# Optimization experiments

Hardware: AMD Instinct MI355X
Metric: run time of the kernel (lower is better)

## Reference

```python
import jax, jax.numpy as jnp
import numpy as np

# dims
B, LP, CIN, AUX = 8, 1024, 64, 32
COUT, OUT_LEN = 64, 512
DM, DI, NS, PH, NH = 1024, 2048, 16, 64, 32  # d_model, d_inner, d_state, headdim, n_heads
NL, PATCH, KPRE, KCONV = 4, 8, 5, 4
GG, KH, CHUNK = 8, 2048, 64  # kan grid, kan hidden, chunk_size
DIN = 2 * DI + 2 * NS + NH   # in_proj output: z, xBC, dt
CONV_DIM = DI + 2 * NS


def _conv1d(x, w, b, stride, pad_l, pad_r, groups=1):
    # x: [B, C, L], w: [O, I/groups, K]
    y = jax.lax.conv_general_dilated(x, w, (stride,), [(pad_l, pad_r)],
                                     dimension_numbers=("NCH", "OIH", "NCH"),
                                     feature_group_count=groups)
    return y + b[None, :, None]


def _rmsnorm(x, w):
    return x * jax.lax.rsqrt(jnp.mean(x * x, axis=-1, keepdims=True) + 1e-5) * w


def _mamba(u, in_w, conv_w, conv_b, A_log, Dh, dt_bias, out_w):
    # Mamba2-style selective SSM block (bias-free projections, causal depthwise conv).
    Bs, L, _ = u.shape
    zxbcdt = jnp.einsum("bld,ed->ble", u, in_w)  # [B,L,DIN]
    z = zxbcdt[..., :DI]
    xBC = zxbcdt[..., DI:DI + CONV_DIM]
    dt = jax.nn.softplus(zxbcdt[..., DI + CONV_DIM:] + dt_bias)  # [B,L,NH]
    xBC = jax.nn.silu(_conv1d(xBC.transpose(0, 2, 1), conv_w, conv_b, 1, KCONV - 1, 0,
                              groups=CONV_DIM)).transpose(0, 2, 1)
    xh = xBC[..., :DI].reshape(Bs, L, NH, PH)
    Bm = xBC[..., DI:DI + NS]   # [B,L,NS]
    Cm = xBC[..., DI + NS:]     # [B,L,NS]
    dA = jnp.exp(-jnp.exp(A_log) * dt)  # [B,L,NH]

    def step(s, t):
        x_t, B_t, C_t, dA_t, dt_t = t
        s = s * dA_t[:, :, None, None] + jnp.einsum("bhp,bn,bh->bhpn", x_t, B_t, dt_t)
        return s, jnp.einsum("bhpn,bn->bhp", s, C_t)

    s0 = jnp.zeros((Bs, NH, PH, NS), u.dtype)
    xs = (xh.transpose(1, 0, 2, 3), Bm.transpose(1, 0, 2), Cm.transpose(1, 0, 2),
          dA.transpose(1, 0, 2), dt.transpose(1, 0, 2))
    _, ys = jax.lax.scan(step, s0, xs)  # ys: [L,B,NH,PH]
    y = ys.transpose(1, 0, 2, 3) + xh * Dh[None, None, :, None]
    y = y.reshape(Bs, L, DI) * jax.nn.silu(z)
    return jnp.einsum("ble,de->bld", y, out_w)


def _kan(x, log_bw, base_w, base_b, spline_w):
    # Gaussian-basis KAN layer: base Linear + spline Linear over RBF expansion.
    grid = jnp.linspace(-2.0, 2.0, GG)
    bw = jnp.exp(log_bw)[None] + 1e-6                 # [1,in,1]
    basis = jnp.exp(-((x[..., None] - grid[None, None, :]) ** 2) / (2.0 * bw * bw))
    return x @ base_w.T + base_b + basis.reshape(x.shape[0], -1) @ spline_w.T


def setup_inputs() -> dict:
    ks = iter(jax.random.split(jax.random.key(0), 64))
    nrm = lambda shape, s=0.02: jax.random.normal(next(ks), shape, jnp.float32) * s
    inp = {"x_prefix": jax.random.normal(next(ks), (B, LP, CIN), jnp.float32),
           "y_aux": jax.random.normal(next(ks), (B, AUX), jnp.float32),
           "pre_conv_w": nrm((DM, CIN, KPRE), 0.1), "pre_conv_b": jnp.zeros((DM,)),
           "patch_w": nrm((DM, DM, PATCH), 0.05), "patch_b": jnp.zeros((DM,))}
    for pre in ("fwd", "bwd"):
        inp[pre + "_norm_w"] = jnp.ones((NL, DM))
        inp[pre + "_in_w"] = nrm((NL, DIN, DM))
        inp[pre + "_conv_w"] = nrm((NL, CONV_DIM, 1, KCONV), 0.1)
        inp[pre + "_conv_b"] = jnp.zeros((NL, CONV_DIM))
        inp[pre + "_A_log"] = jnp.zeros((NL, NH))
        inp[pre + "_D"] = jnp.ones((NL, NH))
        inp[pre + "_dt_bias"] = nrm((NL, NH), 0.5)
        inp[pre + "_out_w"] = nrm((NL, DM, DI))
    inp.update(aux_w=nrm((DM, AUX)), aux_b=jnp.zeros((DM,)),
               kan1_log_bw=jnp.zeros((3 * DM, 1)), kan1_base_w=nrm((KH, 3 * DM)),
               kan1_base_b=jnp.zeros((KH,)), kan1_spline_w=nrm((KH, 3 * DM * GG), 0.005),
               kan2_log_bw=jnp.zeros((KH, 1)), kan2_base_w=nrm((DM, KH)),
               kan2_base_b=jnp.zeros((DM,)), kan2_spline_w=nrm((DM, KH * GG), 0.005),
               shared_w=nrm((DM, DM)), shared_b=jnp.zeros((DM,)),
               heads_w=nrm((COUT, OUT_LEN, DM)), heads_b=jnp.zeros((COUT, OUT_LEN)))
    return inp


def reference(x_prefix, y_aux, pre_conv_w, pre_conv_b, patch_w, patch_b,
              fwd_norm_w, fwd_in_w, fwd_conv_w, fwd_conv_b, fwd_A_log, fwd_D, fwd_dt_bias, fwd_out_w,
              bwd_norm_w, bwd_in_w, bwd_conv_w, bwd_conv_b, bwd_A_log, bwd_D, bwd_dt_bias, bwd_out_w,
              aux_w, aux_b, kan1_log_bw, kan1_base_w, kan1_base_b, kan1_spline_w,
              kan2_log_bw, kan2_base_w, kan2_base_b, kan2_spline_w,
              shared_w, shared_b, heads_w, heads_b):
    # encode_prefix
    x = jax.nn.silu(_conv1d(x_prefix.transpose(0, 2, 1), pre_conv_w, pre_conv_b, 1, KPRE // 2, KPRE // 2))
    x = _conv1d(x, patch_w, patch_b, PATCH, 0, 0).transpose(0, 2, 1)  # [B, 128, DM]
    rem = x.shape[1] % CHUNK
    if rem:
        x = jnp.pad(x, ((0, 0), (0, CHUNK - rem), (0, 0)))
    h_f, h_b = x, x[:, ::-1]
    for i in range(NL):
        h_f = h_f + _mamba(_rmsnorm(h_f, fwd_norm_w[i]), fwd_in_w[i], fwd_conv_w[i], fwd_conv_b[i],
                           fwd_A_log[i], fwd_D[i], fwd_dt_bias[i], fwd_out_w[i])
        h_b = h_b + _mamba(_rmsnorm(h_b, bwd_norm_w[i]), bwd_in_w[i], bwd_conv_w[i], bwd_conv_b[i],
                           bwd_A_log[i], bwd_D[i], bwd_dt_bias[i], bwd_out_w[i])
    ctx = jnp.concatenate([h_f.mean(1), h_b[:, ::-1].mean(1)], axis=-1)  # [B, 2*DM]
    # fusion + heads
    aux = jax.nn.silu(y_aux @ aux_w.T + aux_b)
    fused = jnp.concatenate([ctx, aux], axis=-1)  # [B, 3*DM]
    fused = jax.nn.silu(_kan(fused, kan1_log_bw, kan1_base_w, kan1_base_b, kan1_spline_w))
    fused = jax.nn.silu(_kan(fused, kan2_log_bw, kan2_base_w, kan2_base_b, kan2_spline_w))
    fused = jax.nn.silu(fused @ shared_w.T + shared_b)
    # all channel heads fused into one batched GEMM: [B, OUT_LEN, COUT]
    return jnp.einsum("bd,cld->blc", fused, heads_w) + heads_b.T[None]
```

## Files before the change

### kernel.cpp

```cpp
#include <hip/hip_runtime.h>
#include <hip/hip_bf16.h>
#include <math.h>

#define B_    8
#define LP_   1024
#define CIN_  64
#define DM_   1024
#define DI_   2048
#define NS_   16
#define PH_   64
#define NH_   32
#define NL_   4
#define GG_   8
#define KH_   2048
#define DIN_  4160
#define NPAD_ 4224
#define CONVD_ 2080
#define L_    128
#define R_    1024
#define OUTL_ 512
#define COUT_ 64

typedef __bf16 bf16x8 __attribute__((ext_vector_type(8)));
typedef float f32x4 __attribute__((ext_vector_type(4)));
typedef unsigned short ushort;

__device__ __forceinline__ float silu_f(float x) { return x / (1.0f + expf(-x)); }

__device__ __forceinline__ ushort f2bu(float x) {
    union { __hip_bfloat16 h; ushort u; } c; c.h = __float2bfloat16(x); return c.u;
}
__device__ __forceinline__ float bu2f(ushort u) {
    union { ushort u; __hip_bfloat16 h; } c; c.u = u; return __bfloat162float(c.h);
}

__device__ __forceinline__ void gload_lds16(const void* g, void* l) {
    __builtin_amdgcn_global_load_lds((const __attribute__((address_space(1))) unsigned int*)g,
                                     (__attribute__((address_space(3))) unsigned int*)l, 16, 0, 0);
}

__device__ __forceinline__ float merge2(float a, float b, int mask, int lane) {
    float x = (lane & mask) ? b : a;
    float y = (lane & mask) ? a : b;
    return x + __shfl_xor(y, mask);
}
__device__ __forceinline__ float reduce8(float* a, int lane) {
    float c0 = merge2(a[0], a[1], 1, lane);
    float c1 = merge2(a[2], a[3], 1, lane);
    float c2 = merge2(a[4], a[5], 1, lane);
    float c3 = merge2(a[6], a[7], 1, lane);
    float d0 = merge2(c0, c1, 2, lane);
    float d1 = merge2(c2, c3, 2, lane);
    float e  = merge2(d0, d1, 4, lane);
    e += __shfl_xor(e, 8);
    e += __shfl_xor(e, 16);
    e += __shfl_xor(e, 32);
    return e;
}

#define PREP_W1 327680
#define PREP_W2 8388608
#define PREP_W3 2621440
__global__ __launch_bounds__(256) void k_prep(const float* __restrict__ pre_w, const float* __restrict__ patch_w,
                                              const float* __restrict__ xp,
                                              __hip_bfloat16* __restrict__ wpreT, __hip_bfloat16* __restrict__ wpatchT,
                                              __hip_bfloat16* __restrict__ Apre) {
    int idx = blockIdx.x * 256 + threadIdx.x;
    if (idx < PREP_W1) {
        int d = idx / 320, kk = idx % 320;
        int kp = kk >> 6, c = kk & 63;
        wpreT[idx] = __float2bfloat16(pre_w[(d * CIN_ + c) * 5 + kp]);
    } else if (idx < PREP_W1 + PREP_W2) {
        int i = idx - PREP_W1;
        int d = i >> 13, kk = i & 8191;
        int kp = kk >> 10, din = kk & 1023;
        wpatchT[i] = __float2bfloat16(patch_w[((size_t)d << 13) + din * 8 + kp]);
    } else if (idx < PREP_W1 + PREP_W2 + PREP_W3) {
        int i = idx - PREP_W1 - PREP_W2;
        int kk = i % 320; int r = i / 320;
        int l = r & 1023, b = r >> 10;
        int kp = kk >> 6, c = kk & 63;
        int lp = l + kp - 2;
        float v = 0.f;
        if (lp >= 0 && lp < LP_) v = xp[((size_t)b * LP_ + lp) * CIN_ + c];
        Apre[i] = __float2bfloat16(v);
    }
}

#define CVT_IN_T4  1081344
#define CVT_OUT_T4 524288
#define CVT_PER    1605632
__global__ __launch_bounds__(256) void k_cvt_all(const float* __restrict__ in0, const float* __restrict__ in1,
                                                 const float* __restrict__ o0, const float* __restrict__ o1,
                                                 __hip_bfloat16* __restrict__ wBBa, __hip_bfloat16* __restrict__ wOBa) {
    int i = blockIdx.x * 256 + threadIdx.x;
    if (i >= 8 * CVT_PER) return;
    int ld = i / CVT_PER;
    int r = i - ld * CVT_PER;
    int l = ld >> 1, d = ld & 1;
    const float* inw  = (d ? in1 : in0) + (size_t)l * DIN_ * DM_;
    const float* outw = (d ? o1 : o0) + (size_t)l * DM_ * DI_;
    if (r < CVT_IN_T4) {
        int idx = r * 4; int row = idx >> 10;
        __hip_bfloat16* dst = wBBa + (size_t)ld * NPAD_ * 1024 + idx;
        if (row < DIN_) {
            float4 v = *(const float4*)(inw + idx);
            dst[0] = __float2bfloat16(v.x); dst[1] = __float2bfloat16(v.y);
            dst[2] = __float2bfloat16(v.z); dst[3] = __float2bfloat16(v.w);
        } else {
            dst[0] = __float2bfloat16(0.f); dst[1] = __float2bfloat16(0.f);
            dst[2] = __float2bfloat16(0.f); dst[3] = __float2bfloat16(0.f);
        }
    } else {
        int idx = (r - CVT_IN_T4) * 4;
        __hip_bfloat16* dst = wOBa + (size_t)ld * 2048 * 1024 + idx;
        float4 v = *(const float4*)(outw + idx);
        dst[0] = __float2bfloat16(v.x); dst[1] = __float2bfloat16(v.y);
        dst[2] = __float2bfloat16(v.z); dst[3] = __float2bfloat16(v.w);
    }
}

template<int BM, int BN>
__global__ __launch_bounds__(256) void k_gemm_mfma(
    const ushort* __restrict__ A, const ushort* __restrict__ B,
    const float* __restrict__ bias,
    float* __restrict__ Cf, __hip_bfloat16* __restrict__ Cb,
    int Kc, int ldk, int ldc, int Nstore, int act, int nsplit,
    long sA, long sB, long sC)
{
    constexpr int BK = 32;
    constexpr int WM = BM / 2, WN = BN / 2;
    constexpr int MR = WM / 16, NR = WN / 16;
    constexpr int ACH = BM * 4, BCH = BN * 4;
    __shared__ ushort sAs[2][BM * BK];
    __shared__ ushort sBs[2][BN * BK];
    int tid = threadIdx.x;
    int lane = tid & 63, w = tid >> 6;
    int wr = w >> 1, wc = w & 1;
    int z = blockIdx.z;
    int dir = z / nsplit, ks = z - dir * nsplit;
    int kbase = ks * Kc;
    int m0 = blockIdx.y * BM, n0 = blockIdx.x * BN;
    const ushort* Az = A + (size_t)dir * sA + kbase;
    const ushort* Bz = B + (size_t)dir * sB + kbase;

    auto STAGE = [&](int buf, int k0) {
        #pragma unroll
        for (int c = tid; c < ACH; c += 256) {
            int row = c >> 2, col = (c & 3) * 8;
            gload_lds16(Az + (size_t)(m0 + row) * ldk + k0 + col, (char*)&sAs[buf][0] + c * 16);
        }
        #pragma unroll
        for (int c = tid; c < BCH; c += 256) {
            int row = c >> 2, col = (c & 3) * 8;
            gload_lds16(Bz + (size_t)(n0 + row) * ldk + k0 + col, (char*)&sBs[buf][0] + c * 16);
        }
    };

    f32x4 acc[MR][NR] = {};
    const int NT = Kc / BK;
    STAGE(0, 0);
    __syncthreads();
    int cur = 0;
    for (int t = 0; t < NT; ++t) {
        if (t + 1 < NT) STAGE(cur ^ 1, (t + 1) * BK);
        bf16x8 af[MR], bfr[NR];
        #pragma unroll
        for (int m = 0; m < MR; ++m)
            af[m] = *(const bf16x8*)&sAs[cur][(wr * WM + m * 16 + (lane & 15)) * BK + (lane >> 4) * 8];
        #pragma unroll
        for (int n = 0; n < NR; ++n)
            bfr[n] = *(const bf16x8*)&sBs[cur][(wc * WN + n * 16 + (lane & 15)) * BK + (lane >> 4) * 8];
        #pragma unroll
        for (int m = 0; m < MR; ++m)
            #pragma unroll
            for (int n = 0; n < NR; ++n)
                acc[m][n] = __builtin_amdgcn_mfma_f32_16x16x32_bf16(af[m], bfr[n], acc[m][n], 0, 0, 0);
        __syncthreads();
        cur ^= 1;
    }
    #pragma unroll
    for (int m = 0; m < MR; ++m) {
        int row = m0 + wr * WM + m * 16 + (lane >> 4) * 4;
        #pragma unroll
        for (int n = 0; n < NR; ++n) {
            int col = n0 + wc * WN + n * 16 + (lane & 15);
            if (col < Nstore) {
                if (act == 2) {
                    float* Cfz = Cf + (size_t)z * sC;
                    #pragma unroll
                    for (int j = 0; j < 4; ++j)
                        Cfz[(size_t)(row + j) * ldc + col] = acc[m][n][j];
                } else {
                    __hip_bfloat16* Cbz = Cb + (size_t)dir * sC;
                    float bv = bias ? bias[col] : 0.f;
                    #pragma unroll
                    for (int j = 0; j < 4; ++j) {
                        float v = acc[m][n][j] + bv;
                        if (act == 1) v = silu_f(v);
                        Cbz[(size_t)(row + j) * ldc + col] = __float2bfloat16(v);
                    }
                }
            }
        }
    }
}

__global__ __launch_bounds__(256) void k_patch_fin_rms(const float* __restrict__ part, const float* __restrict__ bias,
                                                       const float* __restrict__ w0, const float* __restrict__ w1,
                                                       float* __restrict__ hf, float* __restrict__ hb,
                                                       __hip_bfloat16* __restrict__ uB) {
    int r = blockIdx.x;
    int t = threadIdx.x;
    int c = t * 4;
    float4 o = *(const float4*)(bias + c);
    #pragma unroll
    for (int s = 0; s < 8; ++s) {
        float4 v = *(const float4*)(part + (size_t)s * 1048576 + ((size_t)r << 10) + c);
        o.x += v.x; o.y += v.y; o.z += v.z; o.w += v.w;
    }
    *(float4*)(hf + ((size_t)r << 10) + c) = o;
    int rb = r ^ 127;
    *(float4*)(hb + ((size_t)rb << 10) + c) = o;
    float ss = o.x * o.x + o.y * o.y + o.z * o.z + o.w * o.w;
    #pragma unroll
    for (int of = 32; of; of >>= 1) ss += __shfl_xor(ss, of);
    __shared__ float sred[4];
    if ((t & 63) == 0) sred[t >> 6] = ss;
    __syncthreads();
    float tot = sred[0] + sred[1] + sred[2] + sred[3];
    float scale = rsqrtf(tot * (1.0f / DM_) + 1e-5f);
    float4 wf = *(const float4*)(w0 + c);
    float4 wb = *(const float4*)(w1 + c);
    __hip_bfloat16* uf = uB + ((size_t)r << 10) + c;
    __hip_bfloat16* ub = uB + ((size_t)(1024 + rb) << 10) + c;
    uf[0] = __float2bfloat16(o.x * scale * wf.x); uf[1] = __float2bfloat16(o.y * scale * wf.y);
    uf[2] = __float2bfloat16(o.z * scale * wf.z); uf[3] = __float2bfloat16(o.w * scale * wf.w);
    ub[0] = __float2bfloat16(o.x * scale * wb.x); ub[1] = __float2bfloat16(o.y * scale * wb.y);
    ub[2] = __float2bfloat16(o.z * scale * wb.z); ub[3] = __float2bfloat16(o.w * scale * wb.w);
}

template<bool DO_RMS>
__global__ __launch_bounds__(256) void k_oproj_fin_rms(const float* __restrict__ part,
                                                       const float* __restrict__ w0, const float* __restrict__ w1,
                                                       float* __restrict__ h, __hip_bfloat16* __restrict__ uB) {
    int row = blockIdx.x;
    int t = threadIdx.x;
    int c = t * 4;
    const float* p = part + (size_t)(row >> 10) * 4194304 + (size_t)(row & 1023) * 1024 + c;
    float4 o = *(const float4*)(h + ((size_t)row << 10) + c);
    #pragma unroll
    for (int s = 0; s < 4; ++s) {
        float4 v = *(const float4*)(p + (size_t)s * 1048576);
        o.x += v.x; o.y += v.y; o.z += v.z; o.w += v.w;
    }
    *(float4*)(h + ((size_t)row << 10) + c) = o;
    if (DO_RMS) {
        float ss = o.x * o.x + o.y * o.y + o.z * o.z + o.w * o.w;
        #pragma unroll
        for (int of = 32; of; of >>= 1) ss += __shfl_xor(ss, of);
        __shared__ float sred[4];
        if ((t & 63) == 0) sred[t >> 6] = ss;
        __syncthreads();
        float tot = sred[0] + sred[1] + sred[2] + sred[3];
        float scale = rsqrtf(tot * (1.0f / DM_) + 1e-5f);
        const float* w = (row >> 10) ? w1 : w0;
        float4 wv = *(const float4*)(w + c);
        __hip_bfloat16* u = uB + ((size_t)row << 10) + c;
        u[0] = __float2bfloat16(o.x * scale * wv.x); u[1] = __float2bfloat16(o.y * scale * wv.y);
        u[2] = __float2bfloat16(o.z * scale * wv.z); u[3] = __float2bfloat16(o.w * scale * wv.w);
    }
}

__global__ __launch_bounds__(256) void k_scan(const __hip_bfloat16* __restrict__ zx,
                                              const float* __restrict__ cw0, const float* __restrict__ cw1,
                                              const float* __restrict__ cb0, const float* __restrict__ cb1,
                                              const float* __restrict__ dtb0, const float* __restrict__ dtb1,
                                              const float* __restrict__ al0, const float* __restrict__ al1,
                                              const float* __restrict__ D0, const float* __restrict__ D1,
                                              __hip_bfloat16* __restrict__ ys) {
    __shared__ float xs[L_ * PH_];
    __shared__ float Bsh[L_ * NS_];
    __shared__ float Csh[L_ * NS_];
    __shared__ float dts[L_];
    __shared__ float dAs[L_];
    int bx = blockIdx.x;
    int dir = bx >> 8, b = (bx >> 5) & 7, h = bx & 31;
    const __hip_bfloat16* zxd = zx + (size_t)dir * 1024 * DIN_;
    const float* cw = dir ? cw1 : cw0;
    const float* cb = dir ? cb1 : cb0;
    const float* dt_bias = dir ? dtb1 : dtb0;
    const float* A_log   = dir ? al1 : al0;
    const float* Dh      = dir ? D1 : D0;
    __hip_bfloat16* ysd  = ys + (size_t)dir * 1024 * DI_;
    int t = threadIdx.x;
    for (int i = t; i < 2048; i += 256) {
        int l = i >> 4, p4 = i & 15;
        int cc = h * PH_ + p4 * 4;
        float a0 = cb[cc + 0], a1 = cb[cc + 1], a2 = cb[cc + 2], a3 = cb[cc + 3];
        #pragma unroll
        for (int k = 0; k < 4; ++k) {
            int lp = l - 3 + k;
            if (lp >= 0) {
                ushort4 raw = *(const ushort4*)(zxd + (size_t)(b * L_ + lp) * DIN_ + DI_ + cc);
                a0 += bu2f(raw.x) * cw[(cc + 0) * 4 + k];
                a1 += bu2f(raw.y) * cw[(cc + 1) * 4 + k];
                a2 += bu2f(raw.z) * cw[(cc + 2) * 4 + k];
                a3 += bu2f(raw.w) * cw[(cc + 3) * 4 + k];
            }
        }
        float* xp = &xs[l * PH_ + p4 * 4];
        xp[0] = silu_f(a0); xp[1] = silu_f(a1); xp[2] = silu_f(a2); xp[3] = silu_f(a3);
    }
    for (int i = t; i < 1024; i += 256) {
        int l = i >> 3, q4 = i & 7;
        int cc = DI_ + q4 * 4;
        float a0 = cb[cc + 0], a1 = cb[cc + 1], a2 = cb[cc + 2], a3 = cb[cc + 3];
        #pragma unroll
        for (int k = 0; k < 4; ++k) {
            int lp = l - 3 + k;
            if (lp >= 0) {
                ushort4 raw = *(const ushort4*)(zxd + (size_t)(b * L_ + lp) * DIN_ + DI_ + cc);
                a0 += bu2f(raw.x) * cw[(cc + 0) * 4 + k];
                a1 += bu2f(raw.y) * cw[(cc + 1) * 4 + k];
                a2 += bu2f(raw.z) * cw[(cc + 2) * 4 + k];
                a3 += bu2f(raw.w) * cw[(cc + 3) * 4 + k];
            }
        }
        float r0 = silu_f(a0), r1 = silu_f(a1), r2 = silu_f(a2), r3 = silu_f(a3);
        if (q4 < 4) {
            float* bp = &Bsh[l * NS_ + q4 * 4];
            bp[0] = r0; bp[1] = r1; bp[2] = r2; bp[3] = r3;
        } else {
            float* cp = &Csh[l * NS_ + (q4 - 4) * 4];
            cp[0] = r0; cp[1] = r1; cp[2] = r2; cp[3] = r3;
        }
    }
    if (t < L_) {
        float v = bu2f(*(const ushort*)(zxd + (size_t)(b * L_ + t) * DIN_ + 4128 + h)) + dt_bias[h];
        float sp = v > 20.f ? v : log1pf(expf(v));
        dts[t] = sp;
        dAs[t] = expf(-expf(A_log[h]) * sp);
    }
    __syncthreads();
    int p = t >> 2, n0 = (t & 3) * 4;
    float Dv = Dh[h];
    float s0 = 0.f, s1 = 0.f, s2 = 0.f, s3 = 0.f;
    for (int l = 0; l < L_; ++l) {
        float x = xs[l * 64 + p];
        float dAv = dAs[l];
        float xdt = x * dts[l];
        s0 = s0 * dAv + xdt * Bsh[l * 16 + n0 + 0];
        s1 = s1 * dAv + xdt * Bsh[l * 16 + n0 + 1];
        s2 = s2 * dAv + xdt * Bsh[l * 16 + n0 + 2];
        s3 = s3 * dAv + xdt * Bsh[l * 16 + n0 + 3];
        float cp = s0 * Csh[l * 16 + n0 + 0] + s1 * Csh[l * 16 + n0 + 1]
                 + s2 * Csh[l * 16 + n0 + 2] + s3 * Csh[l * 16 + n0 + 3];
        cp += __shfl_xor(cp, 1);
        cp += __shfl_xor(cp, 2);
        if ((t & 3) == 0) xs[l * 64 + p] = cp + x * Dv;
    }
    __syncthreads();
    for (int i = t; i < L_ * PH_; i += 256) {
        int l = i >> 6, pp = i & 63;
        float z = bu2f(*(const ushort*)(zxd + (size_t)(b * L_ + l) * DIN_ + h * PH_ + pp));
        ysd[((size_t)(b * L_ + l)) * DI_ + h * PH_ + pp] = __float2bfloat16(xs[i] * silu_f(z));
    }
}

__global__ __launch_bounds__(256) void k_meanctx_aux(const float* __restrict__ hf, const float* __restrict__ hb,
                                                     const float* __restrict__ y_aux, const float* __restrict__ aux_w,
                                                     const float* __restrict__ aux_b, float* __restrict__ fused) {
    int bx = blockIdx.x;
    int t = threadIdx.x;
    if (bx < 64) {
        int b = bx >> 3, ch = bx & 7;
        int d4 = t & 31, lg = t >> 5;
        int d = ch * 128 + d4 * 4;
        float4 sf = {0,0,0,0}, sb = {0,0,0,0};
        for (int l = lg; l < L_; l += 8) {
            float4 a = *(const float4*)(hf + ((size_t)b * L_ + l) * DM_ + d);
            float4 c = *(const float4*)(hb + ((size_t)b * L_ + l) * DM_ + d);
            sf.x += a.x; sf.y += a.y; sf.z += a.z; sf.w += a.w;
            sb.x += c.x; sb.y += c.y; sb.z += c.z; sb.w += c.w;
        }
        __shared__ float rf[8][128], rb[8][128];
        *(float4*)&rf[lg][d4 * 4] = sf;
        *(float4*)&rb[lg][d4 * 4] = sb;
        __syncthreads();
        if (t < 128) {
            float s1 = 0.f, s2 = 0.f;
            #pragma unroll
            for (int g = 0; g < 8; ++g) { s1 += rf[g][t]; s2 += rb[g][t]; }
            fused[b * 3072 + ch * 128 + t] = s1 * (1.f / L_);
            fused[b * 3072 + DM_ + ch * 128 + t] = s2 * (1.f / L_);
        }
    } else {
        int j = (bx - 64) * 256 + t;
        if (j >= DM_) return;
        for (int b = 0; b < B_; ++b) {
            float acc = aux_b[j];
            for (int a = 0; a < 32; ++a) acc += y_aux[b * 32 + a] * aux_w[j * 32 + a];
            fused[b * 3072 + 2 * DM_ + j] = silu_f(acc);
        }
    }
}

__global__ __launch_bounds__(256) void k_basis(const float* __restrict__ x, const float* __restrict__ log_bw,
                                               float* __restrict__ basis, int Din) {
    int idx = blockIdx.x * 256 + threadIdx.x;
    if (idx >= 8 * Din) return;
    int d = idx % Din;
    float xv = x[idx];
    float bw = expf(log_bw[d]) + 1e-6f;
    float inv = 1.0f / (2.0f * bw * bw);
    #pragma unroll
    for (int g = 0; g < GG_; ++g) {
        float gg = -2.0f + g * (4.0f / 7.0f);
        float df = xv - gg;
        basis[(size_t)idx * GG_ + g] = expf(-df * df * inv);
    }
}

template<int MODE>
__global__ __launch_bounds__(256) void k_dotk(const float* __restrict__ Wsp, const float* __restrict__ Xsp, int Ksp,
                                              const float* __restrict__ Wb, const float* __restrict__ Xb, int Kb,
                                              const float* __restrict__ bias, float* __restrict__ out,
                                              int nsp, int nch, int Dout) {
    __shared__ float sX[8][1024];
    int ch = blockIdx.y;
    bool sp = (ch < nsp);
    const float* W = sp ? Wsp : Wb;
    const float* X = sp ? Xsp : Xb;
    int K = sp ? Ksp : Kb;
    int k0 = (sp ? ch : ch - nsp) * 1024;
    int tid = threadIdx.x;
    for (int i = tid; i < 2048; i += 256) {
        int b = i >> 8, kk = (i & 255) * 4;
        *(float4*)&sX[b][kk] = *(const float4*)(X + (size_t)b * K + k0 + kk);
    }
    __syncthreads();
    int wv = tid >> 6, lane = tid & 63;
    int rowBase = blockIdx.x * 32 + wv * 8;
    for (int j = 0; j < 8; ++j) {
        int row = rowBase + j;
        const float* wr = W + (size_t)row * K + k0;
        float acc[8] = {};
        #pragma unroll
        for (int it = 0; it < 4; ++it) {
            int k = it * 256 + lane * 4;
            float4 wvv = *(const float4*)(wr + k);
            #pragma unroll
            for (int b = 0; b < 8; ++b) {
                float4 xv = *(const float4*)&sX[b][k];
                acc[b] += wvv.x * xv.x + wvv.y * xv.y + wvv.z * xv.z + wvv.w * xv.w;
            }
        }
        float e = reduce8(acc, lane);
        if (lane < 8) {
            if (MODE == 0) {
                out[((size_t)row * nch + ch) * 8 + lane] = e;
            } else if (MODE == 1) {
                out[(size_t)lane * Dout + row] = silu_f(e + bias[row]);
            } else {
                int c = row >> 9, l = row & 511;
                out[((size_t)lane * OUTL_ + l) * COUT_ + c] = e + bias[row];
            }
        }
    }
}

__global__ __launch_bounds__(256) void k_fin1_basis2(const float* __restrict__ partial, const float* __restrict__ bb,
                                                     const float* __restrict__ k2_lbw,
                                                     float* __restrict__ k1, float* __restrict__ bas2) {
    int row = blockIdx.x * 256 + threadIdx.x;
    if (row >= 2048) return;
    float bbv = bb[row];
    float lb = expf(k2_lbw[row]) + 1e-6f;
    float inv = 1.0f / (2.0f * lb * lb);
    #pragma unroll
    for (int b = 0; b < 8; ++b) {
        float s = bbv;
        #pragma unroll
        for (int c = 0; c < 27; ++c) s += partial[((size_t)row * 27 + c) * 8 + b];
        float v = silu_f(s);
        k1[(size_t)b * 2048 + row] = v;
        #pragma unroll
        for (int g = 0; g < GG_; ++g) {
            float gg = -2.0f + g * (4.0f / 7.0f);
            float df = v - gg;
            bas2[((size_t)b * 2048 + row) * GG_ + g] = expf(-df * df * inv);
        }
    }
}

template<int NCH>
__global__ __launch_bounds__(256) void k_dot_fin(const float* __restrict__ partial, const float* __restrict__ base_b,
                                                 float* __restrict__ out, int Dout) {
    int row = blockIdx.x * 256 + threadIdx.x;
    if (row >= Dout) return;
    float bb = base_b[row];
    #pragma unroll
    for (int b = 0; b < 8; ++b) {
        float s = bb;
        #pragma unroll
        for (int c = 0; c < NCH; ++c) s += partial[((size_t)row * NCH + c) * 8 + b];
        out[(size_t)b * Dout + row] = silu_f(s);
    }
}

extern "C" void kernel_launch(void* const* d_in, const int* in_sizes, int n_in,
                              void* d_out, int out_size, void* d_ws, size_t ws_size,
                              hipStream_t stream) {
    const float* x_prefix = (const float*)d_in[0];
    const float* y_aux    = (const float*)d_in[1];
    const float* pre_w    = (const float*)d_in[2];
    const float* pre_b    = (const float*)d_in[3];
    const float* patch_w  = (const float*)d_in[4];
    const float* patch_b  = (const float*)d_in[5];
    const float* norm_w[2] = {(const float*)d_in[6],  (const float*)d_in[14]};
    const float* in_w[2]   = {(const float*)d_in[7],  (const float*)d_in[15]};
    const float* conv_w[2] = {(const float*)d_in[8],  (const float*)d_in[16]};
    const float* conv_b[2] = {(const float*)d_in[9],  (const float*)d_in[17]};
    const float* A_log[2]  = {(const float*)d_in[10], (const float*)d_in[18]};
    const float* Dvec[2]   = {(const float*)d_in[11], (const float*)d_in[19]};
    const float* dt_b[2]   = {(const float*)d_in[12], (const float*)d_in[20]};
    const float* out_w[2]  = {(const float*)d_in[13], (const float*)d_in[21]};
    const float* aux_w = (const float*)d_in[22];
    const float* aux_b = (const float*)d_in[23];
    const float* k1_lbw = (const float*)d_in[24];
    const float* k1_bw  = (const float*)d_in[25];
    const float* k1_bb  = (const float*)d_in[26];
    const float* k1_sw  = (const float*)d_in[27];
    const float* k2_lbw = (const float*)d_in[28];
    const float* k2_bw  = (const float*)d_in[29];
    const float* k2_bb  = (const float*)d_in[30];
    const float* k2_sw  = (const float*)d_in[31];
    const float* sh_w = (const float*)d_in[32];
    const float* sh_b = (const float*)d_in[33];
    const float* hw   = (const float*)d_in[34];
    const float* hbias= (const float*)d_in[35];
    float* ws = (float*)d_ws;
    float* out = (float*)d_out;

    const size_t o_ApreB   = 0;
    const size_t o_wpreTB  = 1310720;
    const size_t o_x1B     = 1474560;
    const size_t o_wpatchTB= 5668864;
    const size_t o_uB   = 0;
    const size_t o_zxB  = 1048576;
    const size_t o_ysB  = 5308416;
    const size_t o_hf   = 9863168;
    const size_t o_hb   = 10911744;
    const size_t o_wBBa = 11960320;
    const size_t o_wOBa = 29261824;
    const size_t o_spart= 37650432;
    const size_t total_f = 46039040;
    const size_t o_f1   = 0;
    const size_t o_bas1 = 24576;
    const size_t o_k1   = 221184;
    const size_t o_bas2 = 237568;
    const size_t o_k2   = 368640;
    const size_t o_f4   = 376832;
    const size_t o_part = 385024;
    if (ws_size < total_f * sizeof(float)) return;

    __hip_bfloat16* ApreB   = (__hip_bfloat16*)(ws + o_ApreB);
    __hip_bfloat16* wpreTB  = (__hip_bfloat16*)(ws + o_wpreTB);
    __hip_bfloat16* x1B     = (__hip_bfloat16*)(ws + o_x1B);
    __hip_bfloat16* wpatchTB= (__hip_bfloat16*)(ws + o_wpatchTB);
    __hip_bfloat16* uB      = (__hip_bfloat16*)(ws + o_uB);
    __hip_bfloat16* zxB     = (__hip_bfloat16*)(ws + o_zxB);
    __hip_bfloat16* ysB     = (__hip_bfloat16*)(ws + o_ysB);
    __hip_bfloat16* wBBa    = (__hip_bfloat16*)(ws + o_wBBa);
    __hip_bfloat16* wOBa    = (__hip_bfloat16*)(ws + o_wOBa);
    float* hf = ws + o_hf;
    float* hb = ws + o_hb;

    k_cvt_all<<<50176, 256, 0, stream>>>(in_w[0], in_w[1], out_w[0], out_w[1], wBBa, wOBa);
    k_prep<<<44288, 256, 0, stream>>>(pre_w, patch_w, x_prefix, wpreTB, wpatchTB, ApreB);
    k_gemm_mfma<128,128><<<dim3(8, 64, 1), 256, 0, stream>>>(
        (const ushort*)ApreB, (const ushort*)wpreTB, pre_b, nullptr, x1B,
        320, 320, 1024, 1024, 1, 1, 0, 0, 0);
    k_gemm_mfma<128,128><<<dim3(8, 8, 8), 256, 0, stream>>>(
        (const ushort*)x1B, (const ushort*)wpatchTB, nullptr, ws + o_spart, nullptr,
        1024, 8192, 1024, 1024, 2, 8, 0, 0, (long)1024 * 1024);
    k_patch_fin_rms<<<1024, 256, 0, stream>>>(ws + o_spart, patch_b, norm_w[0], norm_w[1], hf, hb, uB);

    for (int i = 0; i < NL_; ++i) {
        k_gemm_mfma<128,128><<<dim3(33, 8, 2), 256, 0, stream>>>(
            (const ushort*)uB, (const ushort*)(wBBa + (size_t)i * 2 * NPAD_ * 1024), nullptr, nullptr, zxB,
            1024, 1024, DIN_, DIN_, 0, 1, (long)1024 * 1024, (long)NPAD_ * 1024, (long)1024 * DIN_);
        k_scan<<<512, 256, 0, stream>>>(zxB,
            conv_w[0] + (size_t)i * CONVD_ * 4, conv_w[1] + (size_t)i * CONVD_ * 4,
            conv_b[0] + (size_t)i * CONVD_, conv_b[1] + (size_t)i * CONVD_,
            dt_b[0] + i * NH_, dt_b[1] + i * NH_, A_log[0] + i * NH_, A_log[1] + i * NH_,
            Dvec[0] + i * NH_, Dvec[1] + i * NH_, ysB);
        k_gemm_mfma<128,128><<<dim3(8, 8, 8), 256, 0, stream>>>(
            (const ushort*)ysB, (const ushort*)(wOBa + (size_t)i * 2 * 2048 * 1024), nullptr, ws + o_spart, nullptr,
            512, 2048, 1024, 1024, 2, 4, (long)1024 * 2048, (long)2048 * 1024, (long)1024 * 1024);
        if (i + 1 < NL_) {
            k_oproj_fin_rms<true><<<2048, 256, 0, stream>>>(ws + o_spart,
                norm_w[0] + (size_t)(i + 1) * DM_, norm_w[1] + (size_t)(i + 1) * DM_, hf, uB);
        } else {
            k_oproj_fin_rms<false><<<2048, 256, 0, stream>>>(ws + o_spart, nullptr, nullptr, hf, nullptr);
        }
    }

    k_meanctx_aux<<<68, 256, 0, stream>>>(hf, hb, y_aux, aux_w, aux_b, ws + o_f1);
    k_basis<<<96, 256, 0, stream>>>(ws + o_f1, k1_lbw, ws + o_bas1, 3072);
    k_dotk<0><<<dim3(64, 27), 256, 0, stream>>>(k1_sw, ws + o_bas1, 24576, k1_bw, ws + o_f1, 3072,
                                                nullptr, ws + o_part, 24, 27, 2048);
    k_fin1_basis2<<<8, 256, 0, stream>>>(ws + o_part, k1_bb, k2_lbw, ws + o_k1, ws + o_bas2);
    k_dotk<0><<<dim3(32, 18), 256, 0, stream>>>(k2_sw, ws + o_bas2, 16384, k2_bw, ws + o_k1, 2048,
                                                nullptr, ws + o_part, 16, 18, 1024);
    k_dot_fin<18><<<4, 256, 0, stream>>>(ws + o_part, k2_bb, ws + o_k2, 1024);
    k_dotk<1><<<dim3(32, 1), 256, 0, stream>>>(nullptr, nullptr, 0, sh_w, ws + o_k2, 1024,
                                               sh_b, ws + o_f4, 0, 1, 1024);
    k_dotk<2><<<dim3(1024, 1), 256, 0, stream>>>(nullptr, nullptr, 0, hw, ws + o_f4, 1024,
                                                 hbias, out, 0, 1, 32768);
}
```

Baseline: 883.0 us.

## Use 8-wave GEMM blocks and merge weight-conversion and prep kernels

The MFMA GEMM now runs 512 threads per block, with eight waves in a 2x4 layout and 64x32 per-wave sub-tiles in place of four waves covering 64x64 each. This lowers accumulator registers per wave and adds waves per CU to hide latency, at the cost of more LDS-read traffic per block. The separate fp32-to-bf16 weight conversion and prep kernels are fused into one launch to save a kernel launch and its tail. The GEMM change touches every projection in the model.

```diff
diff --git a/kernel.cpp b/kernel.cpp
--- a/kernel.cpp
+++ b/kernel.cpp
@@ -58,14 +58,49 @@
     return e;
 }
 
+#define CVT_IN_T4  1081344
+#define CVT_OUT_T4 524288
+#define CVT_PER    1605632
+#define CVT_TOT    12845056
 #define PREP_W1 327680
 #define PREP_W2 8388608
 #define PREP_W3 2621440
-__global__ __launch_bounds__(256) void k_prep(const float* __restrict__ pre_w, const float* __restrict__ patch_w,
-                                              const float* __restrict__ xp,
-                                              __hip_bfloat16* __restrict__ wpreT, __hip_bfloat16* __restrict__ wpatchT,
-                                              __hip_bfloat16* __restrict__ Apre) {
-    int idx = blockIdx.x * 256 + threadIdx.x;
+#define PREP_TOT 11337728
+__global__ __launch_bounds__(256) void k_cvt_prep(
+    const float* __restrict__ in0, const float* __restrict__ in1,
+    const float* __restrict__ o0, const float* __restrict__ o1,
+    __hip_bfloat16* __restrict__ wBBa, __hip_bfloat16* __restrict__ wOBa,
+    const float* __restrict__ pre_w, const float* __restrict__ patch_w, const float* __restrict__ xp,
+    __hip_bfloat16* __restrict__ wpreT, __hip_bfloat16* __restrict__ wpatchT, __hip_bfloat16* __restrict__ Apre)
+{
+    int gi = blockIdx.x * 256 + threadIdx.x;
+    if (gi < CVT_TOT) {
+        int ld = gi / CVT_PER;
+        int r = gi - ld * CVT_PER;
+        int l = ld >> 1, d = ld & 1;
+        const float* inw  = (d ? in1 : in0) + (size_t)l * DIN_ * DM_;
+        const float* outw = (d ? o1 : o0) + (size_t)l * DM_ * DI_;
+        if (r < CVT_IN_T4) {
+            int idx = r * 4; int row = idx >> 10;
+            __hip_bfloat16* dst = wBBa + (size_t)ld * NPAD_ * 1024 + idx;
+            if (row < DIN_) {
+                float4 v = *(const float4*)(inw + idx);
+                dst[0] = __float2bfloat16(v.x); dst[1] = __float2bfloat16(v.y);
+                dst[2] = __float2bfloat16(v.z); dst[3] = __float2bfloat16(v.w);
+            } else {
+                dst[0] = __float2bfloat16(0.f); dst[1] = __float2bfloat16(0.f);
+                dst[2] = __float2bfloat16(0.f); dst[3] = __float2bfloat16(0.f);
+            }
+        } else {
+            int idx = (r - CVT_IN_T4) * 4;
+            __hip_bfloat16* dst = wOBa + (size_t)ld * 2048 * 1024 + idx;
+            float4 v = *(const float4*)(outw + idx);
+            dst[0] = __float2bfloat16(v.x); dst[1] = __float2bfloat16(v.y);
+            dst[2] = __float2bfloat16(v.z); dst[3] = __float2bfloat16(v.w);
+        }
+        return;
+    }
+    int idx = gi - CVT_TOT;
     if (idx < PREP_W1) {
         int d = idx / 320, kk = idx % 320;
         int kp = kk >> 6, c = kk & 63;
@@ -75,7 +110,7 @@
         int d = i >> 13, kk = i & 8191;
         int kp = kk >> 10, din = kk & 1023;
         wpatchT[i] = __float2bfloat16(patch_w[((size_t)d << 13) + din * 8 + kp]);
-    } else if (idx < PREP_W1 + PREP_W2 + PREP_W3) {
+    } else if (idx < PREP_TOT) {
         int i = idx - PREP_W1 - PREP_W2;
         int kk = i % 320; int r = i / 320;
         int l = r & 1023, b = r >> 10;
@@ -87,41 +122,8 @@
     }
 }
 
-#define CVT_IN_T4  1081344
-#define CVT_OUT_T4 524288
-#define CVT_PER    1605632
-__global__ __launch_bounds__(256) void k_cvt_all(const float* __restrict__ in0, const float* __restrict__ in1,
-                                                 const float* __restrict__ o0, const float* __restrict__ o1,
-                                                 __hip_bfloat16* __restrict__ wBBa, __hip_bfloat16* __restrict__ wOBa) {
-    int i = blockIdx.x * 256 + threadIdx.x;
-    if (i >= 8 * CVT_PER) return;
-    int ld = i / CVT_PER;
-    int r = i - ld * CVT_PER;
-    int l = ld >> 1, d = ld & 1;
-    const float* inw  = (d ? in1 : in0) + (size_t)l * DIN_ * DM_;
-    const float* outw = (d ? o1 : o0) + (size_t)l * DM_ * DI_;
-    if (r < CVT_IN_T4) {
-        int idx = r * 4; int row = idx >> 10;
-        __hip_bfloat16* dst = wBBa + (size_t)ld * NPAD_ * 1024 + idx;
-        if (row < DIN_) {
-            float4 v = *(const float4*)(inw + idx);
-            dst[0] = __float2bfloat16(v.x); dst[1] = __float2bfloat16(v.y);
-            dst[2] = __float2bfloat16(v.z); dst[3] = __float2bfloat16(v.w);
-        } else {
-            dst[0] = __float2bfloat16(0.f); dst[1] = __float2bfloat16(0.f);
-            dst[2] = __float2bfloat16(0.f); dst[3] = __float2bfloat16(0.f);
-        }
-    } else {
-        int idx = (r - CVT_IN_T4) * 4;
-        __hip_bfloat16* dst = wOBa + (size_t)ld * 2048 * 1024 + idx;
-        float4 v = *(const float4*)(outw + idx);
-        dst[0] = __float2bfloat16(v.x); dst[1] = __float2bfloat16(v.y);
-        dst[2] = __float2bfloat16(v.z); dst[3] = __float2bfloat16(v.w);
-    }
-}
-
 template<int BM, int BN>
-__global__ __launch_bounds__(256) void k_gemm_mfma(
+__global__ __launch_bounds__(512) void k_gemm_mfma(
     const ushort* __restrict__ A, const ushort* __restrict__ B,
     const float* __restrict__ bias,
     float* __restrict__ Cf, __hip_bfloat16* __restrict__ Cb,
@@ -129,14 +131,14 @@
     long sA, long sB, long sC)
 {
     constexpr int BK = 32;
-    constexpr int WM = BM / 2, WN = BN / 2;
+    constexpr int WM = 64, WN = 32;
     constexpr int MR = WM / 16, NR = WN / 16;
     constexpr int ACH = BM * 4, BCH = BN * 4;
     __shared__ ushort sAs[2][BM * BK];
     __shared__ ushort sBs[2][BN * BK];
     int tid = threadIdx.x;
     int lane = tid & 63, w = tid >> 6;
-    int wr = w >> 1, wc = w & 1;
+    int wr = w >> 2, wc = w & 3;
     int z = blockIdx.z;
     int dir = z / nsplit, ks = z - dir * nsplit;
     int kbase = ks * Kc;
@@ -146,12 +148,12 @@
 
     auto STAGE = [&](int buf, int k0) {
         #pragma unroll
-        for (int c = tid; c < ACH; c += 256) {
+        for (int c = tid; c < ACH; c += 512) {
             int row = c >> 2, col = (c & 3) * 8;
             gload_lds16(Az + (size_t)(m0 + row) * ldk + k0 + col, (char*)&sAs[buf][0] + c * 16);
         }
         #pragma unroll
-        for (int c = tid; c < BCH; c += 256) {
+        for (int c = tid; c < BCH; c += 512) {
             int row = c >> 2, col = (c & 3) * 8;
             gload_lds16(Bz + (size_t)(n0 + row) * ldk + k0 + col, (char*)&sBs[buf][0] + c * 16);
         }
@@ -577,18 +579,19 @@
     float* hf = ws + o_hf;
     float* hb = ws + o_hb;
 
-    k_cvt_all<<<50176, 256, 0, stream>>>(in_w[0], in_w[1], out_w[0], out_w[1], wBBa, wOBa);
-    k_prep<<<44288, 256, 0, stream>>>(pre_w, patch_w, x_prefix, wpreTB, wpatchTB, ApreB);
-    k_gemm_mfma<128,128><<<dim3(8, 64, 1), 256, 0, stream>>>(
+    k_cvt_prep<<<(CVT_TOT + PREP_TOT + 255) / 256, 256, 0, stream>>>(
+        in_w[0], in_w[1], out_w[0], out_w[1], wBBa, wOBa,
+        pre_w, patch_w, x_prefix, wpreTB, wpatchTB, ApreB);
+    k_gemm_mfma<128,128><<<dim3(8, 64, 1), 512, 0, stream>>>(
         (const ushort*)ApreB, (const ushort*)wpreTB, pre_b, nullptr, x1B,
         320, 320, 1024, 1024, 1, 1, 0, 0, 0);
-    k_gemm_mfma<128,128><<<dim3(8, 8, 8), 256, 0, stream>>>(
+    k_gemm_mfma<128,128><<<dim3(8, 8, 8), 512, 0, stream>>>(
         (const ushort*)x1B, (const ushort*)wpatchTB, nullptr, ws + o_spart, nullptr,
         1024, 8192, 1024, 1024, 2, 8, 0, 0, (long)1024 * 1024);
     k_patch_fin_rms<<<1024, 256, 0, stream>>>(ws + o_spart, patch_b, norm_w[0], norm_w[1], hf, hb, uB);
 
     for (int i = 0; i < NL_; ++i) {
-        k_gemm_mfma<128,128><<<dim3(33, 8, 2), 256, 0, stream>>>(
+        k_gemm_mfma<128,128><<<dim3(33, 8, 2), 512, 0, stream>>>(
             (const ushort*)uB, (const ushort*)(wBBa + (size_t)i * 2 * NPAD_ * 1024), nullptr, nullptr, zxB,
             1024, 1024, DIN_, DIN_, 0, 1, (long)1024 * 1024, (long)NPAD_ * 1024, (long)1024 * DIN_);
         k_scan<<<512, 256, 0, stream>>>(zxB,
@@ -596,7 +599,7 @@
             conv_b[0] + (size_t)i * CONVD_, conv_b[1] + (size_t)i * CONVD_,
             dt_b[0] + i * NH_, dt_b[1] + i * NH_, A_log[0] + i * NH_, A_log[1] + i * NH_,
             Dvec[0] + i * NH_, Dvec[1] + i * NH_, ysB);
-        k_gemm_mfma<128,128><<<dim3(8, 8, 8), 256, 0, stream>>>(
+        k_gemm_mfma<128,128><<<dim3(8, 8, 8), 512, 0, stream>>>(
             (const ushort*)ysB, (const ushort*)(wOBa + (size_t)i * 2 * 2048 * 1024), nullptr, ws + o_spart, nullptr,
             512, 2048, 1024, 1024, 2, 4, (long)1024 * 2048, (long)2048 * 1024, (long)1024 * 1024);
         if (i + 1 < NL_) {
```

After: 856.4 us. 3.0% less time.
